# Optimization experiments

Measured on AMD Instinct MI355X. Metric: run time of the kernel, lower is better.

Reference implementation:

```python
import jax, jax.numpy as jnp
import numpy as np


def setup_inputs() -> dict:
    key = jax.random.key(0)
    k1, k2, k3, k4, k5 = jax.random.split(key, 5)
    B, N, D, H = 4, 1024, 128, 64
    return {
        "embeddings": jax.random.normal(k1, (B, N, D), dtype=jnp.float32),
        "W1": jax.random.normal(k2, (2 * D, H), dtype=jnp.float32) * 0.05,  # Linear(2D -> 64), x@W layout
        "b1": jax.random.normal(k3, (H,), dtype=jnp.float32) * 0.05,
        "W2": jax.random.normal(k4, (H, 1), dtype=jnp.float32) * 0.05,      # Linear(64 -> 1)
        "b2": jax.random.normal(k5, (1,), dtype=jnp.float32) * 0.05,
    }


def reference(embeddings, W1, b1, W2, b2):
    # Original: cat([e_i, e_j]) @ W1 == e_i @ W1[:D] + e_j @ W1[D:]
    # so we compute per-node projections and broadcast-sum, never forming
    # the (B,N,N,2D) concat tensor. Same math, far less traffic.
    B, N, D = embeddings.shape
    Wa, Wb = W1[:D], W1[D:]                      # each (D, 64)
    h_i = jnp.einsum("bnd,dh->bnh", embeddings, Wa)   # (B,N,64)
    h_j = jnp.einsum("bnd,dh->bnh", embeddings, Wb)   # (B,N,64)
    h = jax.nn.relu(h_i[:, :, None, :] + h_j[:, None, :, :] + b1)  # (B,N,N,64)
    scores = jnp.tanh(jnp.einsum("bijh,ho->bijo", h, W2)[..., 0] + b2[0])  # (B,N,N)
    scores = (scores + jnp.swapaxes(scores, 1, 2)) * 0.5  # symmetrize
    return -scores  # complementarity
```

## Files before the change

kernel.cpp:

```cpp
#include <hip/hip_runtime.h>

#define Bb 4
#define Nn 1024
#define Dd 128
#define Hh 64
#define NTILE 16

__device__ __forceinline__ float fast_tanh(float x) {
    const float e = __expf(2.0f * x);
    return __fdividef(e - 1.0f, e + 1.0f);
}

__device__ __forceinline__ int swzA(int row, int cw) {
    return row * Hh + (cw ^ (((row >> 2) & 7) << 2));
}

__global__ __launch_bounds__(512) void proj_kernel(
    const float* __restrict__ emb, const float* __restrict__ W1,
    const float* __restrict__ b1, float* __restrict__ HI2, float* __restrict__ HJ)
{
    __shared__ float se[16][132];
    const int tid = threadIdx.x;
    const int row0 = blockIdx.x * 16;
    {
        const int r = tid >> 5;
        const int c = tid & 31;
        const float4 v = *(const float4*)(emb + (size_t)(row0 + r) * Dd + c * 4);
        *(float4*)&se[r][c * 4] = v;
    }
    __syncthreads();
    const int r  = tid >> 5;
    const int h2 = (tid & 31) * 2;
    float2 acc1 = *(const float2*)(b1 + h2);
    float2 acc2 = make_float2(0.f, 0.f);
    const float* er = se[r];
    #pragma unroll 8
    for (int d = 0; d < Dd; ++d) {
        const float ev = er[d];
        const float2 wa = *(const float2*)(W1 + (size_t)d * Hh + h2);
        const float2 wb = *(const float2*)(W1 + (size_t)(d + Dd) * Hh + h2);
        acc1.x = fmaf(ev, wa.x, acc1.x); acc1.y = fmaf(ev, wa.y, acc1.y);
        acc2.x = fmaf(ev, wb.x, acc2.x); acc2.y = fmaf(ev, wb.y, acc2.y);
    }
    *(float2*)(HI2 + (size_t)(row0 + r) * Hh + h2) = acc1;
    *(float2*)(HJ  + (size_t)(row0 + r) * Hh + h2) = acc2;
}

__global__ __launch_bounds__(256) void score_kernel(
    const float* __restrict__ HI2, const float* __restrict__ HJ,
    const float* __restrict__ W2, float* __restrict__ S)
{
    __shared__ float sA[64 * Hh];
    __shared__ float sB[64 * Hh];
    __shared__ float sW[Hh];

    const int tid = threadIdx.x;
    const int blk = blockIdx.x;
    const int b  = blk >> 8;
    const int p  = blk & 255;
    const int ti = p >> 4;
    const int tj = p & 15;
    const int ri0 = ti * 64, rj0 = tj * 64;

    const float* HIb = HI2 + ((size_t)b * Nn + ri0) * Hh;
    const float* HJb = HJ  + ((size_t)b * Nn + rj0) * Hh;

    if (tid < Hh) sW[tid] = W2[tid];

    #pragma unroll
    for (int k = 0; k < 8; ++k) {
        const int l = tid + k * 256;
        const int panel = l >> 10;
        const int rem   = l & 1023;
        const int row   = rem >> 4;
        const int cw    = (rem & 15) * 4;
        const float4 v = *(const float4*)((panel ? HJb : HIb) + row * Hh + cw);
        float* dst = panel ? sB : sA;
        *(float4*)&dst[swzA(row, cw)] = v;
    }
    __syncthreads();

    const int tx = tid & 15;
    const int ty = tid >> 4;
    const int ar0 = ty * 4, br0 = tx * 4;

    float acc[4][4];
    #pragma unroll
    for (int r = 0; r < 4; ++r)
        #pragma unroll
        for (int c = 0; c < 4; ++c) acc[r][c] = 0.f;

    #pragma unroll 2
    for (int hc = 0; hc < 16; ++hc) {
        const int cw = hc * 4;
        const float4 w = *(const float4*)(sW + cw);
        float4 a[4], bj[4];
        #pragma unroll
        for (int r = 0; r < 4; ++r) a[r]  = *(const float4*)&sA[swzA(ar0 + r, cw)];
        #pragma unroll
        for (int c = 0; c < 4; ++c) bj[c] = *(const float4*)&sB[swzA(br0 + c, cw)];
        #pragma unroll
        for (int r = 0; r < 4; ++r) {
            #pragma unroll
            for (int c = 0; c < 4; ++c) {
                float t;
                t = fmaxf(a[r].x + bj[c].x, 0.f); acc[r][c] = fmaf(t, w.x, acc[r][c]);
                t = fmaxf(a[r].y + bj[c].y, 0.f); acc[r][c] = fmaf(t, w.y, acc[r][c]);
                t = fmaxf(a[r].z + bj[c].z, 0.f); acc[r][c] = fmaf(t, w.z, acc[r][c]);
                t = fmaxf(a[r].w + bj[c].w, 0.f); acc[r][c] = fmaf(t, w.w, acc[r][c]);
            }
        }
    }

    float* Sb = S + (size_t)b * Nn * Nn;
    const int i0 = ri0 + ar0;
    const int j0 = rj0 + br0;
    #pragma unroll
    for (int r = 0; r < 4; ++r) {
        float4 v = make_float4(acc[r][0], acc[r][1], acc[r][2], acc[r][3]);
        *(float4*)(Sb + (size_t)(i0 + r) * Nn + j0) = v;
    }
}

__global__ __launch_bounds__(256) void sym_kernel(
    const float* __restrict__ S, const float* __restrict__ b2p,
    float* __restrict__ out)
{
    __shared__ float bT[64][68];
    const int tid = threadIdx.x;
    const int blk = blockIdx.x;
    const int b  = blk >> 8;
    const int p  = blk & 255;
    const int ti = p >> 4;
    const int tj = p & 15;
    const int i0 = ti * 64, j0 = tj * 64;
    const float* Sb = S + (size_t)b * Nn * Nn;

    #pragma unroll
    for (int k = 0; k < 4; ++k) {
        const int l = tid + k * 256;
        const int jj = l >> 4;
        const int c4 = (l & 15) * 4;
        const float4 v = *(const float4*)(Sb + (size_t)(j0 + jj) * Nn + i0 + c4);
        *(float4*)&bT[jj][c4] = v;
    }
    __syncthreads();

    const float bb = b2p[0];
    const int tx = tid & 15;
    const int ty = tid >> 4;
    float* outb = out + (size_t)b * Nn * Nn;

    #pragma unroll
    for (int r = 0; r < 4; ++r) {
        const int i = ty * 4 + r;
        const float4 a = *(const float4*)(Sb + (size_t)(i0 + i) * Nn + j0 + tx * 4);
        float4 v;
        v.x = -0.5f * (fast_tanh(a.x + bb) + fast_tanh(bT[tx * 4 + 0][i] + bb));
        v.y = -0.5f * (fast_tanh(a.y + bb) + fast_tanh(bT[tx * 4 + 1][i] + bb));
        v.z = -0.5f * (fast_tanh(a.z + bb) + fast_tanh(bT[tx * 4 + 2][i] + bb));
        v.w = -0.5f * (fast_tanh(a.w + bb) + fast_tanh(bT[tx * 4 + 3][i] + bb));
        *(float4*)(outb + (size_t)(i0 + i) * Nn + j0 + tx * 4) = v;
    }
}

extern "C" void kernel_launch(void* const* d_in, const int* in_sizes, int n_in,
                              void* d_out, int out_size, void* d_ws, size_t ws_size,
                              hipStream_t stream) {
    const float* emb = (const float*)d_in[0];
    const float* W1  = (const float*)d_in[1];
    const float* b1  = (const float*)d_in[2];
    const float* W2  = (const float*)d_in[3];
    const float* b2  = (const float*)d_in[4];
    float* out = (float*)d_out;
    float* HI2 = (float*)d_ws;
    float* HJ  = HI2 + (size_t)Bb * Nn * Hh;
    float* S   = HJ  + (size_t)Bb * Nn * Hh;

    proj_kernel<<<(Bb * Nn) / 16, 512, 0, stream>>>(emb, W1, b1, HI2, HJ);
    score_kernel<<<Bb * 256, 256, 0, stream>>>(HI2, HJ, W2, S);
    sym_kernel<<<Bb * 256, 256, 0, stream>>>(S, b2, out);
}
```

Baseline: 118.9 us.

## Use packed FP32 add/FMA in score kernel with 128x64 tiles

Rewrites the score kernel's inner loop to use v_pk_add_f32 and v_pk_fma_f32 inline asm, which process two lanes per instruction. ReLU stays scalar, and the two partial accumulators are summed at the end. The per-block tile doubles to 128 rows of HI, so each thread computes an 8x4 output tile, and the grid is halved. W2 is now read from global memory each iteration instead of shared memory. This targets the VALU-bound inner loop, at the cost of more registers, fewer blocks and the extra shuffles around the packed ops.

```diff
diff --git a/kernel.cpp b/kernel.cpp
--- a/kernel.cpp
+++ b/kernel.cpp
@@ -4,14 +4,25 @@
 #define Nn 1024
 #define Dd 128
 #define Hh 64
-#define NTILE 16
+
+typedef float v2f __attribute__((ext_vector_type(2)));
+typedef float v4f __attribute__((ext_vector_type(4)));
+
+__device__ __forceinline__ v2f pk_add(v2f a, v2f b) {
+    v2f d;
+    asm("v_pk_add_f32 %0, %1, %2" : "=v"(d) : "v"(a), "v"(b));
+    return d;
+}
+__device__ __forceinline__ void pk_fma(v2f& d, v2f a, v2f b) {
+    asm("v_pk_fma_f32 %0, %1, %2, %0" : "+v"(d) : "v"(a), "v"(b));
+}
 
 __device__ __forceinline__ float fast_tanh(float x) {
     const float e = __expf(2.0f * x);
     return __fdividef(e - 1.0f, e + 1.0f);
 }
 
-__device__ __forceinline__ int swzA(int row, int cw) {
+__device__ __forceinline__ int swz(int row, int cw) {
     return row * Hh + (cw ^ (((row >> 2) & 7) << 2));
 }
 
@@ -50,64 +61,88 @@
     const float* __restrict__ HI2, const float* __restrict__ HJ,
     const float* __restrict__ W2, float* __restrict__ S)
 {
-    __shared__ float sA[64 * Hh];
+    __shared__ float sA[128 * Hh];
     __shared__ float sB[64 * Hh];
-    __shared__ float sW[Hh];
 
     const int tid = threadIdx.x;
     const int blk = blockIdx.x;
-    const int b  = blk >> 8;
-    const int p  = blk & 255;
-    const int ti = p >> 4;
-    const int tj = p & 15;
-    const int ri0 = ti * 64, rj0 = tj * 64;
+    const int b   = blk >> 7;
+    const int rem = blk & 127;
+    const int ti  = rem >> 4;
+    const int tj  = rem & 15;
+    const int ri0 = ti * 128, rj0 = tj * 64;
 
     const float* HIb = HI2 + ((size_t)b * Nn + ri0) * Hh;
     const float* HJb = HJ  + ((size_t)b * Nn + rj0) * Hh;
 
-    if (tid < Hh) sW[tid] = W2[tid];
-
-    #pragma unroll
-    for (int k = 0; k < 8; ++k) {
+    #pragma unroll
+    for (int k = 0; k < 12; ++k) {
         const int l = tid + k * 256;
-        const int panel = l >> 10;
-        const int rem   = l & 1023;
-        const int row   = rem >> 4;
-        const int cw    = (rem & 15) * 4;
-        const float4 v = *(const float4*)((panel ? HJb : HIb) + row * Hh + cw);
-        float* dst = panel ? sB : sA;
-        *(float4*)&dst[swzA(row, cw)] = v;
+        if (k < 8) {
+            const int row = l >> 4;
+            const int cw  = (l & 15) * 4;
+            const float4 v = *(const float4*)(HIb + row * Hh + cw);
+            *(float4*)&sA[swz(row, cw)] = v;
+        } else {
+            const int m   = l - 2048;
+            const int row = m >> 4;
+            const int cw  = (m & 15) * 4;
+            const float4 v = *(const float4*)(HJb + row * Hh + cw);
+            *(float4*)&sB[swz(row, cw)] = v;
+        }
     }
     __syncthreads();
 
+    const int ty = tid >> 4;
     const int tx = tid & 15;
-    const int ty = tid >> 4;
-    const int ar0 = ty * 4, br0 = tx * 4;
-
-    float acc[4][4];
-    #pragma unroll
-    for (int r = 0; r < 4; ++r)
+    const int ar0 = ty * 8, br0 = tx * 4;
+
+    int abase[8], axor[8];
+    #pragma unroll
+    for (int r = 0; r < 8; ++r) {
+        abase[r] = (ar0 + r) * Hh;
+        axor[r]  = (((ar0 + r) >> 2) & 7) << 2;
+    }
+    int bbase[4], bxor[4];
+    #pragma unroll
+    for (int c = 0; c < 4; ++c) {
+        bbase[c] = (br0 + c) * Hh;
+        bxor[c]  = (((br0 + c) >> 2) & 7) << 2;
+    }
+
+    v2f acc[8][4];
+    #pragma unroll
+    for (int r = 0; r < 8; ++r)
         #pragma unroll
-        for (int c = 0; c < 4; ++c) acc[r][c] = 0.f;
-
-    #pragma unroll 2
+        for (int c = 0; c < 4; ++c) acc[r][c] = (v2f){0.f, 0.f};
+
+    #pragma unroll 4
     for (int hc = 0; hc < 16; ++hc) {
         const int cw = hc * 4;
-        const float4 w = *(const float4*)(sW + cw);
-        float4 a[4], bj[4];
+        const float4 wv = *(const float4*)(W2 + cw);
+        const v2f w01 = {wv.x, wv.y};
+        const v2f w23 = {wv.z, wv.w};
+
+        v2f blo[4], bhi[4];
         #pragma unroll
-        for (int r = 0; r < 4; ++r) a[r]  = *(const float4*)&sA[swzA(ar0 + r, cw)];
+        for (int c = 0; c < 4; ++c) {
+            const v4f bv = *(const v4f*)&sB[bbase[c] + (cw ^ bxor[c])];
+            blo[c] = __builtin_shufflevector(bv, bv, 0, 1);
+            bhi[c] = __builtin_shufflevector(bv, bv, 2, 3);
+        }
         #pragma unroll
-        for (int c = 0; c < 4; ++c) bj[c] = *(const float4*)&sB[swzA(br0 + c, cw)];
-        #pragma unroll
-        for (int r = 0; r < 4; ++r) {
+        for (int r = 0; r < 8; ++r) {
+            const v4f av = *(const v4f*)&sA[abase[r] + (cw ^ axor[r])];
+            const v2f alo = __builtin_shufflevector(av, av, 0, 1);
+            const v2f ahi = __builtin_shufflevector(av, av, 2, 3);
             #pragma unroll
             for (int c = 0; c < 4; ++c) {
-                float t;
-                t = fmaxf(a[r].x + bj[c].x, 0.f); acc[r][c] = fmaf(t, w.x, acc[r][c]);
-                t = fmaxf(a[r].y + bj[c].y, 0.f); acc[r][c] = fmaf(t, w.y, acc[r][c]);
-                t = fmaxf(a[r].z + bj[c].z, 0.f); acc[r][c] = fmaf(t, w.z, acc[r][c]);
-                t = fmaxf(a[r].w + bj[c].w, 0.f); acc[r][c] = fmaf(t, w.w, acc[r][c]);
+                v2f x0 = pk_add(alo, blo[c]);
+                v2f x1 = pk_add(ahi, bhi[c]);
+                x0.x = fmaxf(x0.x, 0.f); x0.y = fmaxf(x0.y, 0.f);
+                x1.x = fmaxf(x1.x, 0.f); x1.y = fmaxf(x1.y, 0.f);
+                pk_fma(acc[r][c], x0, w01);
+                pk_fma(acc[r][c], x1, w23);
             }
         }
     }
@@ -116,8 +151,12 @@
     const int i0 = ri0 + ar0;
     const int j0 = rj0 + br0;
     #pragma unroll
-    for (int r = 0; r < 4; ++r) {
-        float4 v = make_float4(acc[r][0], acc[r][1], acc[r][2], acc[r][3]);
+    for (int r = 0; r < 8; ++r) {
+        float4 v;
+        v.x = acc[r][0].x + acc[r][0].y;
+        v.y = acc[r][1].x + acc[r][1].y;
+        v.z = acc[r][2].x + acc[r][2].y;
+        v.w = acc[r][3].x + acc[r][3].y;
         *(float4*)(Sb + (size_t)(i0 + r) * Nn + j0) = v;
     }
 }
@@ -178,6 +217,6 @@
     float* S   = HJ  + (size_t)Bb * Nn * Hh;
 
     proj_kernel<<<(Bb * Nn) / 16, 512, 0, stream>>>(emb, W1, b1, HI2, HJ);
-    score_kernel<<<Bb * 256, 256, 0, stream>>>(HI2, HJ, W2, S);
+    score_kernel<<<Bb * 128, 256, 0, stream>>>(HI2, HJ, W2, S);
     sym_kernel<<<Bb * 256, 256, 0, stream>>>(S, b2, out);
 }
```

Measured after the change: 129.3 us. 1.09x slower.
